# Optimization experiments

Measured on AMD Instinct MI355X. Metric: run time of the kernel, lower is better.

## Reference

```python
import jax, jax.numpy as jnp
import numpy as np

N = 50000        # atoms
NEIGH = 12       # neighbors per atom
HID = 128
B = 500          # crystals (100 atoms each, contiguous)
NCLS = 2
BSTEPS, BMIN, BMAX = 40, 0.0, 8.0
ASTEPS, AMIN, AMAX = 10, -1.0, 1.0


def gbf(d, dmin, dmax, steps):
    # Gaussian basis expansion: exp(-(d - mu)^2 / gamma^2)
    filters = jnp.linspace(dmin, dmax, steps)
    gamma = (dmax - dmin) / steps
    return jnp.exp(-(d[..., None] - filters) ** 2 / gamma ** 2)


def sage_conv(x, W_l, b_l, W_r, dst, n):
    # PyG SAGEConv (mean aggr): out[d] = lin_l(mean_{src->d} x[src]) + lin_r(x[d])
    # lin commutes with mean, so project first (N x HID) to avoid a 600k x F gather.
    h = x @ W_l.T                                  # [N, HID]
    h_src = jnp.repeat(h, NEIGH, axis=0)           # source of edge e = e // NEIGH
    s = jax.ops.segment_sum(h_src, dst, num_segments=n)
    cnt = jax.ops.segment_sum(jnp.ones(dst.shape, h.dtype), dst, num_segments=n)
    agg = s / jnp.maximum(cnt, 1.0)[:, None]
    return agg + b_l + x @ W_r.T


def setup_inputs() -> dict:
    key = jax.random.key(0)
    ks = jax.random.split(key, 20)
    inp = {
        "bond_fea": jax.random.uniform(ks[0], (N, NEIGH), jnp.float32) * 8.0,
        "angle_fea": jax.random.uniform(ks[1], (N, NEIGH, NEIGH), jnp.float32) * 2.0 - 1.0,
        "species": jax.random.randint(ks[2], (N,), 0, 100),
        "nbr_idx": jax.random.randint(ks[3], (N, NEIGH), 0, N),
        "crys_idx": jnp.stack([jnp.arange(B) * 100, (jnp.arange(B) + 1) * 100], axis=1),
    }
    def w(k, shape):
        return jax.random.normal(k, shape, jnp.float32) * 0.05
    inp.update({
        "W1b": w(ks[4], (HID, BSTEPS * NEIGH)), "b1b": jnp.zeros((HID,), jnp.float32),
        "W1br": w(ks[5], (HID, BSTEPS * NEIGH)),
        "W1a": w(ks[6], (HID, ASTEPS * NEIGH * NEIGH)), "b1a": jnp.zeros((HID,), jnp.float32),
        "W1ar": w(ks[7], (HID, ASTEPS * NEIGH * NEIGH)),
        "W2b": w(ks[8], (HID, HID)), "b2b": jnp.zeros((HID,), jnp.float32),
        "W2br": w(ks[9], (HID, HID)),
        "W2a": w(ks[10], (HID, HID)), "b2a": jnp.zeros((HID,), jnp.float32),
        "W2ar": w(ks[11], (HID, HID)),
        "Wfc": w(ks[12], (NCLS, 2 * HID)), "bfc": jnp.zeros((NCLS,), jnp.float32),
    })
    return inp


def reference(bond_fea, angle_fea, W1b, b1b, W1br, W1a, b1a, W1ar,
              W2b, b2b, W2br, W2a, b2a, W2ar, Wfc, bfc,
              species, nbr_idx, crys_idx):
    dst = nbr_idx.reshape(-1)                               # [N*NEIGH]
    edge_fea = gbf(bond_fea, BMIN, BMAX, BSTEPS).reshape(N, -1)    # [N, 480]
    angle_f = gbf(angle_fea, AMIN, AMAX, ASTEPS).reshape(N, -1)    # [N, 1440]

    bo = jax.nn.relu(sage_conv(edge_fea, W1b, b1b, W1br, dst, N))
    ao = jax.nn.relu(sage_conv(angle_f, W1a, b1a, W1ar, dst, N))
    # dropout omitted (deterministic eval-mode reference)
    bo = jax.nn.relu(sage_conv(bo, W2b, b2b, W2br, dst, N))
    ao = jax.nn.relu(sage_conv(ao, W2a, b2a, W2ar, dst, N))

    crys_fea = jnp.concatenate([bo, ao], axis=1)            # [N, 256]
    # segment-mean pooling over contiguous [start, end) crystal ranges
    seg = jnp.searchsorted(crys_idx[:, 1], jnp.arange(N), side="right")
    cnt = (crys_idx[:, 1] - crys_idx[:, 0]).astype(crys_fea.dtype)
    pooled = jax.ops.segment_sum(crys_fea, seg, num_segments=B) / cnt[:, None]
    return pooled @ Wfc.T + bfc
```

## Files before the change

### kernel.cpp

```cpp
#include <hip/hip_runtime.h>

#define NEIGHB 12
#define HIDD 128
#define CAP 40

typedef _Float16 half8 __attribute__((ext_vector_type(8)));
typedef float f32x4 __attribute__((ext_vector_type(4)));

__global__ __launch_bounds__(256) void cvt_all(
    const float* __restrict__ W1b, const float* __restrict__ W1br, _Float16* __restrict__ O1b,
    const float* __restrict__ W1a, const float* __restrict__ W1ar, _Float16* __restrict__ O1a,
    const float* __restrict__ W2b, const float* __restrict__ W2br, _Float16* __restrict__ O2b,
    const float* __restrict__ W2a, const float* __restrict__ W2ar, _Float16* __restrict__ O2a) {
    int blk = blockIdx.x;
    const float *Wl, *Wr; _Float16* out; int K, Kp, base;
    if (blk < 512)       { Wl = W1b; Wr = W1br; out = O1b; K = 480;  Kp = 512;  base = 0; }
    else if (blk < 1984) { Wl = W1a; Wr = W1ar; out = O1a; K = 1440; Kp = 1472; base = 512; }
    else if (blk < 2112) { Wl = W2b; Wr = W2br; out = O2b; K = 128;  Kp = 128;  base = 1984; }
    else                 { Wl = W2a; Wr = W2ar; out = O2a; K = 128;  Kp = 128;  base = 2112; }
    int idx = (blk - base) * 256 + threadIdx.x;
    int n = idx / Kp, k = idx - n * Kp;
    float v = 0.f;
    if (k < K) v = (n < HIDD) ? Wl[(size_t)n * K + k] : Wr[(size_t)(n - HIDD) * K + k];
    out[idx] = (_Float16)v;
}

template <int MODE, int KTOT, int KP>
__global__ __launch_bounds__(256) void gemm_f16(
    const void* __restrict__ Ain, const _Float16* __restrict__ Wt,
    _Float16* __restrict__ Cl, _Float16* __restrict__ Cr, int rows) {
    constexpr int SUB  = (MODE == 2) ? 10 : 40;
    constexpr int RAWC = (MODE == 2) ? 144 : 12;
    constexpr float MU0 = (MODE == 2) ? -1.0f : 0.0f;
    constexpr float DMU = (MODE == 2) ? (2.0f / 9.0f) : (8.0f / 39.0f);
    constexpr int NT = KP / 64;

    __shared__ __align__(16) _Float16 As[64 * 64];
    __shared__ __align__(16) _Float16 Bs[256 * 64];

    const int tid = threadIdx.x;
    const int lane = tid & 63;
    const int wave = tid >> 6;
    const int iBase = blockIdx.x * 64;
    const int mrow = tid >> 3;
    const int g = tid & 7;
    const int g8 = g * 8;

    const int gi0 = min(iBase + mrow, rows - 1);
    const int gi1 = min(iBase + mrow + 32, rows - 1);
    const _Float16* Ap = (const _Float16*)Ain;
    const float* rr0 = (const float*)Ain + (size_t)gi0 * RAWC;
    const float* rr1 = (const float*)Ain + (size_t)gi1 * RAWC;

    half8 bReg[8];
    half8 aExp[2];
    float r0v[2], r1v[2];

#define PREFETCH(KC)                                                              \
    {                                                                             \
        _Pragma("unroll")                                                         \
        for (int q = 0; q < 8; ++q)                                               \
            bReg[q] = *reinterpret_cast<const half8*>(                            \
                Wt + (size_t)(mrow + 32 * q) * KP + (KC) + g8);                   \
        if (MODE == 0) {                                                          \
            aExp[0] = *reinterpret_cast<const half8*>(Ap + (size_t)gi0 * KP + (KC) + g8); \
            aExp[1] = *reinterpret_cast<const half8*>(Ap + (size_t)gi1 * KP + (KC) + g8); \
        } else {                                                                  \
            int k0 = (KC) + g8;                                                   \
            if (k0 < KTOT) {                                                      \
                int j0 = k0 / SUB;                                                \
                r0v[0] = rr0[j0]; r0v[1] = rr1[j0];                               \
                if (MODE == 2) {                                                  \
                    int jn = min(j0 + 1, RAWC - 1);                               \
                    r1v[0] = rr0[jn]; r1v[1] = rr1[jn];                           \
                }                                                                 \
            }                                                                     \
        }                                                                         \
    }

#define EXPAND(KC)                                                                \
    if (MODE != 0) {                                                              \
        int k0 = (KC) + g8;                                                       \
        if (k0 < KTOT) {                                                          \
            int j0 = k0 / SUB, t0 = k0 - j0 * SUB;                                \
            _Pragma("unroll")                                                     \
            for (int q = 0; q < 2; ++q) {                                         \
                float ra = r0v[q];                                                \
                float rb = (MODE == 2) ? r1v[q] : r0v[q];                         \
                half8 v;                                                          \
                _Pragma("unroll")                                                 \
                for (int e2 = 0; e2 < 8; ++e2) {                                  \
                    int tt = t0 + e2;                                             \
                    bool c2 = (tt >= SUB);                                        \
                    float dd = (c2 ? rb : ra) -                                   \
                               (MU0 + (float)(c2 ? tt - SUB : tt) * DMU);         \
                    v[e2] = (_Float16)__expf(-25.f * dd * dd);                    \
                }                                                                 \
                aExp[q] = v;                                                      \
            }                                                                     \
        } else {                                                                  \
            _Pragma("unroll")                                                     \
            for (int q = 0; q < 2; ++q) {                                         \
                half8 v;                                                          \
                _Pragma("unroll")                                                 \
                for (int e2 = 0; e2 < 8; ++e2) v[e2] = (_Float16)0.f;             \
                aExp[q] = v;                                                      \
            }                                                                     \
        }                                                                         \
    }

    f32x4 acc[4][4];
#pragma unroll
    for (int a = 0; a < 4; ++a)
#pragma unroll
        for (int b = 0; b < 4; ++b)
#pragma unroll
            for (int r = 0; r < 4; ++r) acc[a][b][r] = 0.f;

    PREFETCH(0);
    EXPAND(0);

#pragma unroll 1
    for (int t = 0; t < NT; ++t) {
        const int kc = t * 64;
        __syncthreads();
#pragma unroll
        for (int q = 0; q < 2; ++q) {
            int m = mrow + 32 * q;
            *reinterpret_cast<half8*>(As + m * 64 + ((g ^ (m & 7)) << 3)) = aExp[q];
        }
#pragma unroll
        for (int q = 0; q < 8; ++q) {
            int n = mrow + 32 * q;
            *reinterpret_cast<half8*>(Bs + n * 64 + ((g ^ (n & 7)) << 3)) = bReg[q];
        }
        __syncthreads();
        const bool hasNext = (t + 1) < NT;
        if (hasNext) PREFETCH(kc + 64);
#pragma unroll
        for (int s = 0; s < 2; ++s) {
            int cg = s * 4 + (lane >> 4);
            half8 af[4], bf[4];
#pragma unroll
            for (int a = 0; a < 4; ++a) {
                int m = a * 16 + (lane & 15);
                af[a] = *reinterpret_cast<const half8*>(As + m * 64 + ((cg ^ (m & 7)) << 3));
            }
#pragma unroll
            for (int b = 0; b < 4; ++b) {
                int n = wave * 64 + b * 16 + (lane & 15);
                bf[b] = *reinterpret_cast<const half8*>(Bs + n * 64 + ((cg ^ (n & 7)) << 3));
            }
#pragma unroll
            for (int a = 0; a < 4; ++a)
#pragma unroll
                for (int b = 0; b < 4; ++b)
                    acc[a][b] = __builtin_amdgcn_mfma_f32_16x16x32_f16(af[a], bf[b], acc[a][b], 0, 0, 0);
        }
        if (hasNext) EXPAND(kc + 64);
    }
#undef PREFETCH
#undef EXPAND

    _Float16* Cout = (wave < 2) ? Cl : Cr;
    int nBase = (wave & 1) * 64;
#pragma unroll
    for (int a = 0; a < 4; ++a) {
        int mrel = a * 16 + ((lane >> 4) << 2);
#pragma unroll
        for (int r = 0; r < 4; ++r) {
            int m = iBase + mrel + r;
            if (m < rows) {
#pragma unroll
                for (int b = 0; b < 4; ++b) {
                    int n = nBase + b * 16 + (lane & 15);
                    Cout[(size_t)m * HIDD + n] = (_Float16)acc[a][b][r];
                }
            }
        }
    }
}

__global__ void build_inc(const int* __restrict__ nbr, int* __restrict__ cnt,
                          int* __restrict__ inc, int nEdges) {
    int e = blockIdx.x * blockDim.x + threadIdx.x;
    if (e >= nEdges) return;
    int d = nbr[e];
    int src = e / NEIGHB;
    int pos = atomicAdd(&cnt[d], 1);
    if (pos < CAP) inc[(size_t)d * CAP + pos] = src;
}

__global__ __launch_bounds__(256) void agg2(
    const _Float16* __restrict__ Hbl, const _Float16* __restrict__ Hbr,
    const _Float16* __restrict__ Hal, const _Float16* __restrict__ Har,
    const int* __restrict__ cnt, const int* __restrict__ inc,
    const float* __restrict__ biasB, const float* __restrict__ biasA,
    _Float16* __restrict__ Ob, _Float16* __restrict__ Oa, int N) {
    int d = blockIdx.x * 16 + (threadIdx.x >> 4);
    if (d >= N) return;
    int c8 = (threadIdx.x & 15) * 8;
    int c = cnt[d];
    int cc = min(c, CAP);
    const int* lst = inc + (size_t)d * CAP;
    int4 q0 = *reinterpret_cast<const int4*>(lst);
    int4 q1 = *reinterpret_cast<const int4*>(lst + 4);
    int4 q2 = *reinterpret_cast<const int4*>(lst + 8);
    int idx[12] = {q0.x, q0.y, q0.z, q0.w, q1.x, q1.y, q1.z, q1.w,
                   q2.x, q2.y, q2.z, q2.w};
    half8 vb[12], va[12];
#pragma unroll
    for (int e = 0; e < 12; ++e) {
        int ii = (e < cc) ? idx[e] : 0;
        vb[e] = *reinterpret_cast<const half8*>(Hbl + (size_t)ii * HIDD + c8);
        va[e] = *reinterpret_cast<const half8*>(Hal + (size_t)ii * HIDD + c8);
    }
    float sb[8], sa[8];
#pragma unroll
    for (int j = 0; j < 8; ++j) { sb[j] = 0.f; sa[j] = 0.f; }
#pragma unroll
    for (int e = 0; e < 12; ++e) {
        float w = (e < cc) ? 1.f : 0.f;
#pragma unroll
        for (int j = 0; j < 8; ++j) {
            sb[j] = fmaf(w, (float)vb[e][j], sb[j]);
            sa[j] = fmaf(w, (float)va[e][j], sa[j]);
        }
    }
    for (int e = 12; e < cc; ++e) {
        int ii = lst[e];
        half8 xb = *reinterpret_cast<const half8*>(Hbl + (size_t)ii * HIDD + c8);
        half8 xa = *reinterpret_cast<const half8*>(Hal + (size_t)ii * HIDD + c8);
#pragma unroll
        for (int j = 0; j < 8; ++j) { sb[j] += (float)xb[j]; sa[j] += (float)xa[j]; }
    }
    float inv = 1.f / (float)max(c, 1);
    half8 rb = *reinterpret_cast<const half8*>(Hbr + (size_t)d * HIDD + c8);
    half8 ra = *reinterpret_cast<const half8*>(Har + (size_t)d * HIDD + c8);
    float4 bb0 = *reinterpret_cast<const float4*>(biasB + c8);
    float4 bb1 = *reinterpret_cast<const float4*>(biasB + c8 + 4);
    float4 ba0 = *reinterpret_cast<const float4*>(biasA + c8);
    float4 ba1 = *reinterpret_cast<const float4*>(biasA + c8 + 4);
    float fb[8] = {bb0.x, bb0.y, bb0.z, bb0.w, bb1.x, bb1.y, bb1.z, bb1.w};
    float fa[8] = {ba0.x, ba0.y, ba0.z, ba0.w, ba1.x, ba1.y, ba1.z, ba1.w};
    half8 ob, oa;
#pragma unroll
    for (int j = 0; j < 8; ++j) {
        ob[j] = (_Float16)fmaxf(sb[j] * inv + fb[j] + (float)rb[j], 0.f);
        oa[j] = (_Float16)fmaxf(sa[j] * inv + fa[j] + (float)ra[j], 0.f);
    }
    *reinterpret_cast<half8*>(Ob + (size_t)d * HIDD + c8) = ob;
    *reinterpret_cast<half8*>(Oa + (size_t)d * HIDD + c8) = oa;
}

__global__ __launch_bounds__(256) void pool_fc(const _Float16* __restrict__ bo,
                                               const _Float16* __restrict__ ao,
                                               const int* __restrict__ crys,
                                               const float* __restrict__ Wfc,
                                               const float* __restrict__ bfc,
                                               float* __restrict__ out) {
    __shared__ float red0[256];
    __shared__ float red1[256];
    int b = blockIdx.x;
    int t = threadIdx.x;
    int s0 = crys[b * 2 + 0];
    int s1 = crys[b * 2 + 1];
    const _Float16* src = (t < HIDD) ? bo : ao;
    int col = t & (HIDD - 1);
    float s = 0.f;
    for (int i = s0; i < s1; ++i) s += (float)src[(size_t)i * HIDD + col];
    float pooled = s / (float)(s1 - s0);
    red0[t] = pooled * Wfc[t];
    red1[t] = pooled * Wfc[256 + t];
    __syncthreads();
    for (int off = 128; off >= 1; off >>= 1) {
        if (t < off) {
            red0[t] += red0[t + off];
            red1[t] += red1[t + off];
        }
        __syncthreads();
    }
    if (t == 0) {
        out[b * 2 + 0] = red0[0] + bfc[0];
        out[b * 2 + 1] = red1[0] + bfc[1];
    }
}

extern "C" void kernel_launch(void* const* d_in, const int* in_sizes, int n_in,
                              void* d_out, int out_size, void* d_ws, size_t ws_size,
                              hipStream_t stream) {
    const float* bond = (const float*)d_in[0];
    const float* angle = (const float*)d_in[1];
    const int* nbr = (const int*)d_in[3];
    const int* crys = (const int*)d_in[4];
    const float* W1b = (const float*)d_in[5];
    const float* b1b = (const float*)d_in[6];
    const float* W1br = (const float*)d_in[7];
    const float* W1a = (const float*)d_in[8];
    const float* b1a = (const float*)d_in[9];
    const float* W1ar = (const float*)d_in[10];
    const float* W2b = (const float*)d_in[11];
    const float* b2b = (const float*)d_in[12];
    const float* W2br = (const float*)d_in[13];
    const float* W2a = (const float*)d_in[14];
    const float* b2a = (const float*)d_in[15];
    const float* W2ar = (const float*)d_in[16];
    const float* Wfc = (const float*)d_in[17];
    const float* bfc = (const float*)d_in[18];
    float* out = (float*)d_out;

    const int N = in_sizes[2];
    const int B = in_sizes[4] / 2;
    const int nEdges = N * NEIGHB;

    char* p = (char*)d_ws;
    _Float16* Hbl = (_Float16*)p;  p += (size_t)N * HIDD * 2;
    _Float16* Hbr = (_Float16*)p;  p += (size_t)N * HIDD * 2;
    _Float16* Hal = (_Float16*)p;  p += (size_t)N * HIDD * 2;
    _Float16* Har = (_Float16*)p;  p += (size_t)N * HIDD * 2;
    _Float16* bo  = (_Float16*)p;  p += (size_t)N * HIDD * 2;
    _Float16* ao  = (_Float16*)p;  p += (size_t)N * HIDD * 2;
    _Float16* bo2 = (_Float16*)p;  p += (size_t)N * HIDD * 2;
    _Float16* ao2 = (_Float16*)p;  p += (size_t)N * HIDD * 2;
    int* cnt = (int*)p;            p += (size_t)N * 4;
    int* inc = (int*)p;            p += (size_t)N * CAP * 4;
    _Float16* W1bp = (_Float16*)p; p += 256 * 512 * 2;
    _Float16* W1ap = (_Float16*)p; p += 256 * 1472 * 2;
    _Float16* W2bp = (_Float16*)p; p += 256 * 128 * 2;
    _Float16* W2ap = (_Float16*)p;

    hipMemsetAsync(cnt, 0, (size_t)N * 4, stream);
    build_inc<<<(nEdges + 255) / 256, 256, 0, stream>>>(nbr, cnt, inc, nEdges);
    cvt_all<<<2240, 256, 0, stream>>>(W1b, W1br, W1bp, W1a, W1ar, W1ap,
                                      W2b, W2br, W2bp, W2a, W2ar, W2ap);

    const int gB = (N + 63) / 64;
    const int aB = (N + 15) / 16;

    gemm_f16<1, 480, 512><<<gB, 256, 0, stream>>>(bond, W1bp, Hbl, Hbr, N);
    gemm_f16<2, 1440, 1472><<<gB, 256, 0, stream>>>(angle, W1ap, Hal, Har, N);
    agg2<<<aB, 256, 0, stream>>>(Hbl, Hbr, Hal, Har, cnt, inc, b1b, b1a, bo, ao, N);
    gemm_f16<0, 128, 128><<<gB, 256, 0, stream>>>(bo, W2bp, Hbl, Hbr, N);
    gemm_f16<0, 128, 128><<<gB, 256, 0, stream>>>(ao, W2ap, Hal, Har, N);
    agg2<<<aB, 256, 0, stream>>>(Hbl, Hbr, Hal, Har, cnt, inc, b2b, b2a, bo2, ao2, N);

    pool_fc<<<B, 256, 0, stream>>>(bo2, ao2, crys, Wfc, bfc, out);
}
```

Baseline: 411.4 us.

## Pre-pack weights into MFMA fragment layout, double-buffer A tile, merge GEMM launches

Measured after the change: 410.8 us. No clear change (-0.1%).

```diff
diff --git a/kernel.cpp b/kernel.cpp
--- a/kernel.cpp
+++ b/kernel.cpp
@@ -7,7 +7,7 @@
 typedef _Float16 half8 __attribute__((ext_vector_type(8)));
 typedef float f32x4 __attribute__((ext_vector_type(4)));
 
-__global__ __launch_bounds__(256) void cvt_all(
+__global__ __launch_bounds__(256) void cvt_pack(
     const float* __restrict__ W1b, const float* __restrict__ W1br, _Float16* __restrict__ O1b,
     const float* __restrict__ W1a, const float* __restrict__ W1ar, _Float16* __restrict__ O1a,
     const float* __restrict__ W2b, const float* __restrict__ W2br, _Float16* __restrict__ O2b,
@@ -22,26 +22,27 @@
     int n = idx / Kp, k = idx - n * Kp;
     float v = 0.f;
     if (k < K) v = (n < HIDD) ? Wl[(size_t)n * K + k] : Wr[(size_t)(n - HIDD) * K + k];
-    out[idx] = (_Float16)v;
+    int t = k >> 6, s = (k >> 5) & 1, g = (k >> 3) & 3, e = k & 7;
+    int nb = n >> 4, col = n & 15;
+    size_t addr = ((((size_t)t * 16 + nb) * 2 + s) * 64 + (g * 16 + col)) * 8 + e;
+    out[addr] = (_Float16)v;
 }
 
 template <int MODE, int KTOT, int KP>
-__global__ __launch_bounds__(256) void gemm_f16(
-    const void* __restrict__ Ain, const _Float16* __restrict__ Wt,
-    _Float16* __restrict__ Cl, _Float16* __restrict__ Cr, int rows) {
+__device__ __forceinline__ void gemm_body(
+    const void* __restrict__ Ain, const _Float16* __restrict__ Wp,
+    _Float16* __restrict__ Cl, _Float16* __restrict__ Cr,
+    int rows, int mb, _Float16* As) {
     constexpr int SUB  = (MODE == 2) ? 10 : 40;
     constexpr int RAWC = (MODE == 2) ? 144 : 12;
     constexpr float MU0 = (MODE == 2) ? -1.0f : 0.0f;
     constexpr float DMU = (MODE == 2) ? (2.0f / 9.0f) : (8.0f / 39.0f);
     constexpr int NT = KP / 64;
 
-    __shared__ __align__(16) _Float16 As[64 * 64];
-    __shared__ __align__(16) _Float16 Bs[256 * 64];
-
     const int tid = threadIdx.x;
     const int lane = tid & 63;
     const int wave = tid >> 6;
-    const int iBase = blockIdx.x * 64;
+    const int iBase = mb * 64;
     const int mrow = tid >> 3;
     const int g = tid & 7;
     const int g8 = g * 8;
@@ -52,21 +53,26 @@
     const float* rr0 = (const float*)Ain + (size_t)gi0 * RAWC;
     const float* rr1 = (const float*)Ain + (size_t)gi1 * RAWC;
 
-    half8 bReg[8];
-    half8 aExp[2];
+    half8 bA[8], bB[8], aExp[2];
     float r0v[2], r1v[2];
 
-#define PREFETCH(KC)                                                              \
+#define PREFB(T, DST)                                                             \
     {                                                                             \
         _Pragma("unroll")                                                         \
-        for (int q = 0; q < 8; ++q)                                               \
-            bReg[q] = *reinterpret_cast<const half8*>(                            \
-                Wt + (size_t)(mrow + 32 * q) * KP + (KC) + g8);                   \
+        for (int q = 0; q < 8; ++q) {                                             \
+            int s_ = q >> 2, b_ = q & 3;                                          \
+            (DST)[q] = *reinterpret_cast<const half8*>(                           \
+                Wp + ((((size_t)(T) * 16 + (wave * 4 + b_)) * 2 + s_) * 64 + lane) * 8); \
+        }                                                                         \
+    }
+
+#define LOADA(T)                                                                  \
+    {                                                                             \
         if (MODE == 0) {                                                          \
-            aExp[0] = *reinterpret_cast<const half8*>(Ap + (size_t)gi0 * KP + (KC) + g8); \
-            aExp[1] = *reinterpret_cast<const half8*>(Ap + (size_t)gi1 * KP + (KC) + g8); \
+            aExp[0] = *reinterpret_cast<const half8*>(Ap + (size_t)gi0 * KP + (T) * 64 + g8); \
+            aExp[1] = *reinterpret_cast<const half8*>(Ap + (size_t)gi1 * KP + (T) * 64 + g8); \
         } else {                                                                  \
-            int k0 = (KC) + g8;                                                   \
+            int k0 = (T) * 64 + g8;                                               \
             if (k0 < KTOT) {                                                      \
                 int j0 = k0 / SUB;                                                \
                 r0v[0] = rr0[j0]; r0v[1] = rr1[j0];                               \
@@ -78,9 +84,9 @@
         }                                                                         \
     }
 
-#define EXPAND(KC)                                                                \
+#define EXPAND(T)                                                                 \
     if (MODE != 0) {                                                              \
-        int k0 = (KC) + g8;                                                       \
+        int k0 = (T) * 64 + g8;                                                   \
         if (k0 < KTOT) {                                                          \
             int j0 = k0 / SUB, t0 = k0 - j0 * SUB;                                \
             _Pragma("unroll")                                                     \
@@ -109,6 +115,46 @@
         }                                                                         \
     }
 
+#define WRAS(BUF)                                                                 \
+    {                                                                             \
+        _Pragma("unroll")                                                         \
+        for (int q = 0; q < 2; ++q) {                                             \
+            int m_ = mrow + 32 * q;                                               \
+            *reinterpret_cast<half8*>(As + (BUF) * 4096 + m_ * 64 +               \
+                                      ((g ^ (m_ & 7)) << 3)) = aExp[q];           \
+        }                                                                         \
+    }
+
+#define COMPUTE(BUF, BREG)                                                        \
+    {                                                                             \
+        _Pragma("unroll")                                                         \
+        for (int s_ = 0; s_ < 2; ++s_) {                                          \
+            int cg = s_ * 4 + (lane >> 4);                                        \
+            half8 af[4];                                                          \
+            _Pragma("unroll")                                                     \
+            for (int a_ = 0; a_ < 4; ++a_) {                                      \
+                int m_ = a_ * 16 + (lane & 15);                                   \
+                af[a_] = *reinterpret_cast<const half8*>(                         \
+                    As + (BUF) * 4096 + m_ * 64 + ((cg ^ (m_ & 7)) << 3));        \
+            }                                                                     \
+            _Pragma("unroll")                                                     \
+            for (int a_ = 0; a_ < 4; ++a_)                                        \
+                _Pragma("unroll")                                                 \
+                for (int b_ = 0; b_ < 4; ++b_)                                    \
+                    acc[a_][b_] = __builtin_amdgcn_mfma_f32_16x16x32_f16(         \
+                        af[a_], (BREG)[s_ * 4 + b_], acc[a_][b_], 0, 0, 0);       \
+        }                                                                         \
+    }
+
+#define STEP(T, BCUR, BNEXT)                                                      \
+    {                                                                             \
+        __syncthreads();                                                          \
+        const bool hn = (T) + 1 < NT;                                             \
+        if (hn) { PREFB((T) + 1, BNEXT); LOADA((T) + 1); }                        \
+        COMPUTE((T) & 1, BCUR);                                                   \
+        if (hn) { EXPAND((T) + 1); WRAS(((T) + 1) & 1); }                         \
+    }
+
     f32x4 acc[4][4];
 #pragma unroll
     for (int a = 0; a < 4; ++a)
@@ -117,50 +163,22 @@
 #pragma unroll
             for (int r = 0; r < 4; ++r) acc[a][b][r] = 0.f;
 
-    PREFETCH(0);
+    PREFB(0, bA);
+    LOADA(0);
     EXPAND(0);
+    WRAS(0);
 
 #pragma unroll 1
-    for (int t = 0; t < NT; ++t) {
-        const int kc = t * 64;
-        __syncthreads();
-#pragma unroll
-        for (int q = 0; q < 2; ++q) {
-            int m = mrow + 32 * q;
-            *reinterpret_cast<half8*>(As + m * 64 + ((g ^ (m & 7)) << 3)) = aExp[q];
-        }
-#pragma unroll
-        for (int q = 0; q < 8; ++q) {
-            int n = mrow + 32 * q;
-            *reinterpret_cast<half8*>(Bs + n * 64 + ((g ^ (n & 7)) << 3)) = bReg[q];
-        }
-        __syncthreads();
-        const bool hasNext = (t + 1) < NT;
-        if (hasNext) PREFETCH(kc + 64);
-#pragma unroll
-        for (int s = 0; s < 2; ++s) {
-            int cg = s * 4 + (lane >> 4);
-            half8 af[4], bf[4];
-#pragma unroll
-            for (int a = 0; a < 4; ++a) {
-                int m = a * 16 + (lane & 15);
-                af[a] = *reinterpret_cast<const half8*>(As + m * 64 + ((cg ^ (m & 7)) << 3));
-            }
-#pragma unroll
-            for (int b = 0; b < 4; ++b) {
-                int n = wave * 64 + b * 16 + (lane & 15);
-                bf[b] = *reinterpret_cast<const half8*>(Bs + n * 64 + ((cg ^ (n & 7)) << 3));
-            }
-#pragma unroll
-            for (int a = 0; a < 4; ++a)
-#pragma unroll
-                for (int b = 0; b < 4; ++b)
-                    acc[a][b] = __builtin_amdgcn_mfma_f32_16x16x32_f16(af[a], bf[b], acc[a][b], 0, 0, 0);
-        }
-        if (hasNext) EXPAND(kc + 64);
-    }
-#undef PREFETCH
+    for (int t = 0; t < NT; t += 2) {
+        STEP(t, bA, bB);
+        if (t + 1 < NT) STEP(t + 1, bB, bA);
+    }
+#undef PREFB
+#undef LOADA
 #undef EXPAND
+#undef WRAS
+#undef COMPUTE
+#undef STEP
 
     _Float16* Cout = (wave < 2) ? Cl : Cr;
     int nBase = (wave & 1) * 64;
@@ -179,6 +197,30 @@
             }
         }
     }
+}
+
+__global__ __launch_bounds__(256) void gemm_l1(
+    const float* __restrict__ bond, const _Float16* __restrict__ Wb,
+    _Float16* __restrict__ Hbl, _Float16* __restrict__ Hbr,
+    const float* __restrict__ angle, const _Float16* __restrict__ Wa,
+    _Float16* __restrict__ Hal, _Float16* __restrict__ Har, int rows, int aGB) {
+    __shared__ __align__(16) _Float16 As[2 * 64 * 64];
+    if ((int)blockIdx.x < aGB)
+        gemm_body<2, 1440, 1472>(angle, Wa, Hal, Har, rows, blockIdx.x, As);
+    else
+        gemm_body<1, 480, 512>(bond, Wb, Hbl, Hbr, rows, blockIdx.x - aGB, As);
+}
+
+__global__ __launch_bounds__(256) void gemm_l2(
+    const _Float16* __restrict__ bo, const _Float16* __restrict__ Wb,
+    _Float16* __restrict__ Hbl, _Float16* __restrict__ Hbr,
+    const _Float16* __restrict__ ao, const _Float16* __restrict__ Wa,
+    _Float16* __restrict__ Hal, _Float16* __restrict__ Har, int rows) {
+    __shared__ __align__(16) _Float16 As[2 * 64 * 64];
+    if (blockIdx.y == 0)
+        gemm_body<0, 128, 128>(bo, Wb, Hbl, Hbr, rows, blockIdx.x, As);
+    else
+        gemm_body<0, 128, 128>(ao, Wa, Hal, Har, rows, blockIdx.x, As);
 }
 
 __global__ void build_inc(const int* __restrict__ nbr, int* __restrict__ cnt,
@@ -331,17 +373,17 @@
 
     hipMemsetAsync(cnt, 0, (size_t)N * 4, stream);
     build_inc<<<(nEdges + 255) / 256, 256, 0, stream>>>(nbr, cnt, inc, nEdges);
-    cvt_all<<<2240, 256, 0, stream>>>(W1b, W1br, W1bp, W1a, W1ar, W1ap,
-                                      W2b, W2br, W2bp, W2a, W2ar, W2ap);
+    cvt_pack<<<2240, 256, 0, stream>>>(W1b, W1br, W1bp, W1a, W1ar, W1ap,
+                                       W2b, W2br, W2bp, W2a, W2ar, W2ap);
 
     const int gB = (N + 63) / 64;
     const int aB = (N + 15) / 16;
 
-    gemm_f16<1, 480, 512><<<gB, 256, 0, stream>>>(bond, W1bp, Hbl, Hbr, N);
-    gemm_f16<2, 1440, 1472><<<gB, 256, 0, stream>>>(angle, W1ap, Hal, Har, N);
+    gemm_l1<<<gB * 2, 256, 0, stream>>>(bond, W1bp, Hbl, Hbr,
+                                        angle, W1ap, Hal, Har, N, gB);
     agg2<<<aB, 256, 0, stream>>>(Hbl, Hbr, Hal, Har, cnt, inc, b1b, b1a, bo, ao, N);
-    gemm_f16<0, 128, 128><<<gB, 256, 0, stream>>>(bo, W2bp, Hbl, Hbr, N);
-    gemm_f16<0, 128, 128><<<gB, 256, 0, stream>>>(ao, W2ap, Hal, Har, N);
+    gemm_l2<<<dim3(gB, 2), 256, 0, stream>>>(bo, W2bp, Hbl, Hbr,
+                                             ao, W2ap, Hal, Har, N);
     agg2<<<aB, 256, 0, stream>>>(Hbl, Hbr, Hal, Har, cnt, inc, b2b, b2a, bo2, ao2, N);
 
     pool_fc<<<B, 256, 0, stream>>>(bo2, ao2, crys, Wfc, bfc, out);
```
